# Kernel optimization log

Hardware: AMD Instinct MI355X
Metric: run time of the kernel (lower is better)

Reference implementation:

```python
import jax, jax.numpy as jnp
import numpy as np

B, C, H, W = 4, 512, 64, 64
RED = 8
D = max(1, C // RED)  # inter_channels = 64
BN_EPS = 1e-5


def conv1x1(x, w, b):
    # x: [B,Cin,H,W], w: [Cout,Cin], b: [Cout]
    return jnp.einsum('oc,bchw->bohw', w, x) + b[None, :, None, None]


def setup_inputs() -> dict:
    key = jax.random.key(0)
    ks = jax.random.split(key, 12)
    s = 0.02
    return {
        'x': jax.random.normal(ks[0], (B, C, H, W), jnp.float32),
        'theta_w': jax.random.normal(ks[1], (D, C), jnp.float32) * s,
        'theta_b': jax.random.normal(ks[2], (D,), jnp.float32) * s,
        'phi_w': jax.random.normal(ks[3], (D, C), jnp.float32) * s,
        'phi_b': jax.random.normal(ks[4], (D,), jnp.float32) * s,
        'g_w': jax.random.normal(ks[5], (D, C), jnp.float32) * s,
        'g_b': jax.random.normal(ks[6], (D,), jnp.float32) * s,
        'out_w': jax.random.normal(ks[7], (C, D), jnp.float32) * s,
        'out_b': jax.random.normal(ks[8], (C,), jnp.float32) * s,
        'bn_gamma': jnp.ones((C,), jnp.float32),
        'bn_beta': jnp.zeros((C,), jnp.float32),
        'scale': jax.random.normal(ks[9], (1,), jnp.float32) * 0.1,
    }


def reference(x, theta_w, theta_b, phi_w, phi_b, g_w, g_b,
              out_w, out_b, bn_gamma, bn_beta, scale):
    b, c, h, w = x.shape
    n = h * w
    theta = conv1x1(x, theta_w, theta_b).reshape(b, D, n)  # [B,D,N]
    phi = conv1x1(x, phi_w, phi_b).reshape(b, D, n)        # [B,D,N]
    g = conv1x1(x, g_w, g_b).reshape(b, D, n)              # [B,D,N]
    # attention[b,i,j] = sum_d theta[b,d,i] * phi[b,d,j] (unscaled)
    attn = jax.nn.softmax(jnp.einsum('bdi,bdj->bij', theta, phi), axis=-1)
    # y[b,d,i] = sum_j g[b,d,j] * attn[b,i,j]
    y = jnp.einsum('bdj,bij->bdi', g, attn).reshape(b, D, h, w)
    y = conv1x1(y, out_w, out_b)  # [B,C,H,W]
    # BatchNorm2d, training-mode batch statistics over (B,H,W)
    mean = jnp.mean(y, axis=(0, 2, 3), keepdims=True)
    var = jnp.var(y, axis=(0, 2, 3), keepdims=True)
    y = (y - mean) * jax.lax.rsqrt(var + BN_EPS)
    y = y * bn_gamma[None, :, None, None] + bn_beta[None, :, None, None]
    return x + scale.reshape(()) * y
```

## Files before the change

### kernel.cpp

```cpp
#include <hip/hip_runtime.h>
#include <hip/hip_bf16.h>
#include <math.h>

#define NPIX 4096
#define CIN  512
#define DD   64
#define BB   4
#define NCHUNK 8

using f32x4  = __attribute__((ext_vector_type(4))) float;
using bf16x8 = __attribute__((ext_vector_type(8))) short;
using u16x4  = __attribute__((ext_vector_type(4))) unsigned short;

__device__ __forceinline__ unsigned short f2bf(float f){
    union { __hip_bfloat16 h; unsigned short u; } v;
    v.h = __float2bfloat16(f);
    return v.u;
}

__device__ __forceinline__ float bf2f(unsigned short u){
    union { unsigned u; float f; } v; v.u = ((unsigned)u) << 16; return v.f;
}

__device__ __forceinline__ unsigned pk2(float a, float b){
    union { __hip_bfloat162 h; unsigned u; } v;
    v.h = __float22bfloat162_rn(make_float2(a, b));
    return v.u;
}

__device__ __forceinline__ bf16x8 cvt8(float4 a, float4 b){
    union { unsigned u[4]; bf16x8 v; } r;
    r.u[0] = pk2(a.x, a.y); r.u[1] = pk2(a.z, a.w);
    r.u[2] = pk2(b.x, b.y); r.u[3] = pk2(b.z, b.w);
    return r.v;
}

__global__ __launch_bounds__(256) void k0_xt(
    const float* __restrict__ x, unsigned short* __restrict__ xT)
{
    const int n0 = blockIdx.x * 64;
    const int c0 = blockIdx.y * 64;
    const int b  = blockIdx.z;
    const int tid = threadIdx.x;
    __shared__ __align__(16) unsigned short T[64*72];

    {
        const int kr = tid >> 2, ns = (tid & 3) * 16;
        const float* xp = x + ((size_t)b*CIN + c0 + kr)*NPIX + n0 + ns;
        float4 a0 = *reinterpret_cast<const float4*>(xp);
        float4 a1 = *reinterpret_cast<const float4*>(xp + 4);
        float4 a2 = *reinterpret_cast<const float4*>(xp + 8);
        float4 a3 = *reinterpret_cast<const float4*>(xp + 12);
        *reinterpret_cast<bf16x8*>(&T[kr*72 + ns])     = cvt8(a0, a1);
        *reinterpret_cast<bf16x8*>(&T[kr*72 + ns + 8]) = cvt8(a2, a3);
    }
    __syncthreads();
    {
        const int nr = tid >> 2, ks = (tid & 3) * 16;
        unsigned short v[16];
        #pragma unroll
        for (int i=0;i<16;++i) v[i] = T[(ks+i)*72 + nr];
        unsigned short* dst = xT + ((size_t)b*NPIX + n0 + nr)*CIN + c0 + ks;
        *reinterpret_cast<bf16x8*>(dst)     = *reinterpret_cast<bf16x8*>(&v[0]);
        *reinterpret_cast<bf16x8*>(dst + 8) = *reinterpret_cast<bf16x8*>(&v[8]);
    }
}

__global__ __launch_bounds__(256, 4) void k1_qkv(
    const unsigned short* __restrict__ xT,
    const float* __restrict__ tw, const float* __restrict__ tbv,
    const float* __restrict__ pw, const float* __restrict__ pbv,
    const float* __restrict__ gw, const float* __restrict__ gbv,
    unsigned short* __restrict__ thetaT, unsigned short* __restrict__ phiT,
    unsigned short* __restrict__ g_dn)
{
    const int n0 = blockIdx.x * 64;
    const int kt = blockIdx.y;
    const int b  = blockIdx.z;
    const int tid = threadIdx.x;
    const float* W  = (kt==0) ? tw  : (kt==1) ? pw  : gw;
    const float* Bv = (kt==0) ? tbv : (kt==1) ? pbv : gbv;
    const float wsc = (kt==0) ? 1.4426950408889634f : 1.0f;

    const int wq   = tid >> 6;
    const int lane = tid & 63;
    const int lr   = lane & 15;
    const int lg   = lane >> 4;

    __shared__ __align__(16) short Wt[64*72];
    __shared__ __align__(16) short Xt[64*72];

    f32x4 acc[4];
    #pragma unroll
    for (int jt=0;jt<4;++jt) acc[jt] = (f32x4){0.f,0.f,0.f,0.f};

    const int srow = tid >> 2;
    const int skq  = (tid & 3) * 16;

    for (int k0 = 0; k0 < CIN; k0 += 64) {
        __syncthreads();
        {
            const float* wp = W + (size_t)srow*CIN + k0 + skq;
            float4 w0 = *reinterpret_cast<const float4*>(wp);
            float4 w1 = *reinterpret_cast<const float4*>(wp + 4);
            float4 w2 = *reinterpret_cast<const float4*>(wp + 8);
            float4 w3 = *reinterpret_cast<const float4*>(wp + 12);
            w0.x*=wsc; w0.y*=wsc; w0.z*=wsc; w0.w*=wsc;
            w1.x*=wsc; w1.y*=wsc; w1.z*=wsc; w1.w*=wsc;
            w2.x*=wsc; w2.y*=wsc; w2.z*=wsc; w2.w*=wsc;
            w3.x*=wsc; w3.y*=wsc; w3.z*=wsc; w3.w*=wsc;
            *reinterpret_cast<bf16x8*>(&Wt[srow*72 + skq])     = cvt8(w0, w1);
            *reinterpret_cast<bf16x8*>(&Wt[srow*72 + skq + 8]) = cvt8(w2, w3);
            const unsigned short* xp = xT + ((size_t)b*NPIX + n0 + srow)*CIN + k0 + skq;
            *reinterpret_cast<bf16x8*>(&Xt[srow*72 + skq]) =
                *reinterpret_cast<const bf16x8*>(xp);
            *reinterpret_cast<bf16x8*>(&Xt[srow*72 + skq + 8]) =
                *reinterpret_cast<const bf16x8*>(xp + 8);
        }
        __syncthreads();

        __builtin_amdgcn_s_setprio(1);
        #pragma unroll
        for (int dc=0;dc<2;++dc){
            bf16x8 af = *reinterpret_cast<const bf16x8*>(&Wt[(wq*16+lr)*72 + dc*32 + lg*8]);
            #pragma unroll
            for (int jt=0;jt<4;++jt){
                bf16x8 bf = *reinterpret_cast<const bf16x8*>(&Xt[(jt*16+lr)*72 + dc*32 + lg*8]);
                acc[jt] = __builtin_amdgcn_mfma_f32_16x16x32_bf16(af, bf, acc[jt], 0,0,0);
            }
        }
        __builtin_amdgcn_s_setprio(0);
    }

    const int mb = wq*16 + lg*4;
    float bv[4];
    #pragma unroll
    for (int r=0;r<4;++r) bv[r] = Bv[mb+r] * wsc;

    if (kt < 2){
        unsigned short* dst = (kt==0) ? thetaT : phiT;
        #pragma unroll
        for (int jt=0;jt<4;++jt){
            union { unsigned u[2]; u16x4 v; } o;
            o.u[0] = pk2(acc[jt][0]+bv[0], acc[jt][1]+bv[1]);
            o.u[1] = pk2(acc[jt][2]+bv[2], acc[jt][3]+bv[3]);
            *reinterpret_cast<u16x4*>(&dst[((size_t)b*NPIX + n0 + jt*16+lr)*DD + mb]) = o.v;
        }
    } else {
        #pragma unroll
        for (int jt=0;jt<4;++jt)
            #pragma unroll
            for (int r=0;r<4;++r)
                g_dn[((size_t)b*DD + mb+r)*NPIX + n0 + jt*16+lr] = f2bf(acc[jt][r]+bv[r]);
    }
}

__global__ __launch_bounds__(256, 4) void k2_attn(
    const unsigned short* __restrict__ thetaT,
    const unsigned short* __restrict__ phiT,
    const unsigned short* __restrict__ g_dn,
    unsigned short* __restrict__ pY, float* __restrict__ pL)
{
    const int i0 = blockIdx.x * 128;
    const int ch = blockIdx.y;
    const int b  = blockIdx.z;
    const int tid  = threadIdx.x;
    const int wq   = tid >> 6;
    const int lane = tid & 63;
    const int lr   = lane & 15;
    const int lg   = lane >> 4;

    __shared__ __align__(16) short Kt[64*72];
    __shared__ __align__(16) short Gt[64*72];
    __shared__ __align__(16) short Pb[4*32*72];
    short* Pw = &Pb[wq*32*72];

    bf16x8 qf0[2], qf1[2];
    {
        const unsigned short* qp0 = thetaT + ((size_t)b*NPIX + i0 + wq*16 + lr)*DD + lg*8;
        qf0[0] = *reinterpret_cast<const bf16x8*>(qp0);
        qf0[1] = *reinterpret_cast<const bf16x8*>(qp0 + 32);
        const unsigned short* qp1 = qp0 + (size_t)64*DD;
        qf1[0] = *reinterpret_cast<const bf16x8*>(qp1);
        qf1[1] = *reinterpret_cast<const bf16x8*>(qp1 + 32);
    }
    const bf16x8 onesf = { (short)0x3F80,(short)0x3F80,(short)0x3F80,(short)0x3F80,
                           (short)0x3F80,(short)0x3F80,(short)0x3F80,(short)0x3F80 };

    f32x4 yacc0[4], yacc1[4], lacc0, lacc1;
    #pragma unroll
    for (int dt=0;dt<4;++dt){
        yacc0[dt] = (f32x4){0.f,0.f,0.f,0.f};
        yacc1[dt] = (f32x4){0.f,0.f,0.f,0.f};
    }
    lacc0 = (f32x4){0.f,0.f,0.f,0.f};
    lacc1 = (f32x4){0.f,0.f,0.f,0.f};

    const unsigned short* phb = phiT + (size_t)b*NPIX*DD;
    const unsigned short* gb  = g_dn + (size_t)b*DD*NPIX;

    const int jbeg = ch * (NPIX / NCHUNK);
    const int jend = jbeg + (NPIX / NCHUNK);

    const int srow = tid >> 3;
    const int scb  = (tid & 7) * 8;

    for (int j0 = jbeg; j0 < jend; j0 += 64) {
        __syncthreads();
        *reinterpret_cast<float4*>(&Kt[srow*72 + scb]) =
            *reinterpret_cast<const float4*>(&phb[(size_t)(j0+srow)*DD + scb]);
        *reinterpret_cast<float4*>(&Kt[(srow+32)*72 + scb]) =
            *reinterpret_cast<const float4*>(&phb[(size_t)(j0+srow+32)*DD + scb]);
        *reinterpret_cast<float4*>(&Gt[srow*72 + scb]) =
            *reinterpret_cast<const float4*>(&gb[(size_t)srow*NPIX + j0 + scb]);
        *reinterpret_cast<float4*>(&Gt[(srow+32)*72 + scb]) =
            *reinterpret_cast<const float4*>(&gb[(size_t)(srow+32)*NPIX + j0 + scb]);
        __syncthreads();

        f32x4 s0[4], s1[4];
        #pragma unroll
        for (int jt=0;jt<4;++jt){
            s0[jt] = (f32x4){0.f,0.f,0.f,0.f};
            s1[jt] = (f32x4){0.f,0.f,0.f,0.f};
        }
        __builtin_amdgcn_s_setprio(1);
        #pragma unroll
        for (int dc=0;dc<2;++dc){
            #pragma unroll
            for (int jt=0;jt<4;++jt){
                bf16x8 bf = *reinterpret_cast<const bf16x8*>(&Kt[(jt*16+lr)*72 + dc*32 + lg*8]);
                s0[jt] = __builtin_amdgcn_mfma_f32_16x16x32_bf16(qf0[dc], bf, s0[jt], 0,0,0);
                s1[jt] = __builtin_amdgcn_mfma_f32_16x16x32_bf16(qf1[dc], bf, s1[jt], 0,0,0);
            }
        }
        __builtin_amdgcn_s_setprio(0);

        #pragma unroll
        for (int jt=0;jt<4;++jt)
            #pragma unroll
            for (int r=0;r<4;++r){
                Pw[(lg*4+r)*72      + jt*16 + lr] = (short)f2bf(exp2f(fminf(s0[jt][r], 86.f)));
                Pw[(16+lg*4+r)*72   + jt*16 + lr] = (short)f2bf(exp2f(fminf(s1[jt][r], 86.f)));
            }

        __builtin_amdgcn_s_setprio(1);
        #pragma unroll
        for (int jc=0;jc<2;++jc){
            bf16x8 af0 = *reinterpret_cast<const bf16x8*>(&Pw[lr*72      + jc*32 + lg*8]);
            bf16x8 af1 = *reinterpret_cast<const bf16x8*>(&Pw[(16+lr)*72 + jc*32 + lg*8]);
            #pragma unroll
            for (int dt=0;dt<4;++dt){
                bf16x8 gf = *reinterpret_cast<const bf16x8*>(&Gt[(dt*16+lr)*72 + jc*32 + lg*8]);
                yacc0[dt] = __builtin_amdgcn_mfma_f32_16x16x32_bf16(af0, gf, yacc0[dt], 0,0,0);
                yacc1[dt] = __builtin_amdgcn_mfma_f32_16x16x32_bf16(af1, gf, yacc1[dt], 0,0,0);
            }
            lacc0 = __builtin_amdgcn_mfma_f32_16x16x32_bf16(af0, onesf, lacc0, 0,0,0);
            lacc1 = __builtin_amdgcn_mfma_f32_16x16x32_bf16(af1, onesf, lacc1, 0,0,0);
        }
        __builtin_amdgcn_s_setprio(0);
    }

    {
        unsigned short* py0 = pY + (((size_t)b*NCHUNK + ch)*NPIX + i0 + wq*16)*DD;
        unsigned short* py1 = py0 + (size_t)64*DD;
        #pragma unroll
        for (int r=0;r<4;++r)
            #pragma unroll
            for (int dt=0;dt<4;++dt){
                py0[(size_t)(lg*4+r)*DD + dt*16 + lr] = f2bf(yacc0[dt][r]);
                py1[(size_t)(lg*4+r)*DD + dt*16 + lr] = f2bf(yacc1[dt][r]);
            }
        if (lr == 0){
            const size_t base = ((size_t)b*NCHUNK + ch)*NPIX + i0 + wq*16;
            #pragma unroll
            for (int r=0;r<4;++r){
                pL[base + lg*4+r]      = lacc0[r];
                pL[base + 64 + lg*4+r] = lacc1[r];
            }
        }
    }
}

__global__ __launch_bounds__(256) void k2c_combine(
    const unsigned short* __restrict__ pY, const float* __restrict__ pL,
    unsigned short* __restrict__ yTb)
{
    const int gid = blockIdx.x*256 + threadIdx.x;
    const int d2 = gid & 31;
    const int qn = gid >> 5;
    const int b  = qn >> 12;
    const int i  = qn & (NPIX-1);

    float lsum = 0.f, y0 = 0.f, y1 = 0.f;
    #pragma unroll
    for (int c=0;c<NCHUNK;++c){
        lsum += pL[((size_t)b*NCHUNK + c)*NPIX + i];
        ushort2 v = *reinterpret_cast<const ushort2*>(
            &pY[(((size_t)b*NCHUNK + c)*NPIX + i)*DD + d2*2]);
        y0 += bf2f(v.x); y1 += bf2f(v.y);
    }
    float inv = 1.f / lsum;
    *reinterpret_cast<unsigned*>(&yTb[(size_t)qn*DD + d2*2]) = pk2(y0*inv, y1*inv);
}

__global__ __launch_bounds__(256) void k3_out(
    const unsigned short* __restrict__ yTb, const float* __restrict__ ow,
    const float* __restrict__ ob, float* __restrict__ y2,
    float* __restrict__ psum, float* __restrict__ qsum)
{
    const int n0 = blockIdx.x * 64;
    const int c0 = blockIdx.y * 64;
    const int b  = blockIdx.z;
    const int tid = threadIdx.x;
    const int wq   = tid >> 6;
    const int lane = tid & 63;
    const int lr   = lane & 15;
    const int lg   = lane >> 4;

    __shared__ __align__(16) short Ot[64*72];
    __shared__ __align__(16) short Yt[64*72];

    {
        const int srow = tid >> 2, skq = (tid & 3) * 16;
        const float* wp = ow + (size_t)(c0+srow)*DD + skq;
        float4 w0 = *reinterpret_cast<const float4*>(wp);
        float4 w1 = *reinterpret_cast<const float4*>(wp + 4);
        float4 w2 = *reinterpret_cast<const float4*>(wp + 8);
        float4 w3 = *reinterpret_cast<const float4*>(wp + 12);
        *reinterpret_cast<bf16x8*>(&Ot[srow*72 + skq])     = cvt8(w0, w1);
        *reinterpret_cast<bf16x8*>(&Ot[srow*72 + skq + 8]) = cvt8(w2, w3);
        const unsigned short* yp = yTb + ((size_t)b*NPIX + n0 + srow)*DD + skq;
        *reinterpret_cast<bf16x8*>(&Yt[srow*72 + skq]) =
            *reinterpret_cast<const bf16x8*>(yp);
        *reinterpret_cast<bf16x8*>(&Yt[srow*72 + skq + 8]) =
            *reinterpret_cast<const bf16x8*>(yp + 8);
    }
    __syncthreads();

    f32x4 acc[4];
    #pragma unroll
    for (int jt=0;jt<4;++jt) acc[jt] = (f32x4){0.f,0.f,0.f,0.f};
    #pragma unroll
    for (int dc=0;dc<2;++dc){
        bf16x8 af = *reinterpret_cast<const bf16x8*>(&Ot[(wq*16+lr)*72 + dc*32 + lg*8]);
        #pragma unroll
        for (int jt=0;jt<4;++jt){
            bf16x8 bf = *reinterpret_cast<const bf16x8*>(&Yt[(jt*16+lr)*72 + dc*32 + lg*8]);
            acc[jt] = __builtin_amdgcn_mfma_f32_16x16x32_bf16(af, bf, acc[jt], 0,0,0);
        }
    }

    const int cb = c0 + wq*16 + lg*4;
    float bv[4];
    #pragma unroll
    for (int r=0;r<4;++r) bv[r] = ob[cb+r];

    float sr[4] = {0,0,0,0}, qr[4] = {0,0,0,0};
    #pragma unroll
    for (int jt=0;jt<4;++jt)
        #pragma unroll
        for (int r=0;r<4;++r){
            float v = acc[jt][r] + bv[r];
            y2[((size_t)b*CIN + cb+r)*NPIX + n0 + jt*16+lr] = v;
            sr[r] += v; qr[r] += v*v;
        }
    #pragma unroll
    for (int off=1; off<16; off<<=1)
        #pragma unroll
        for (int r=0;r<4;++r){
            sr[r] += __shfl_xor(sr[r], off);
            qr[r] += __shfl_xor(qr[r], off);
        }
    if (lr == 0){
        const int slot = b*64 + blockIdx.x;
        #pragma unroll
        for (int r=0;r<4;++r){
            psum[(size_t)(cb+r)*256 + slot] = sr[r];
            qsum[(size_t)(cb+r)*256 + slot] = qr[r];
        }
    }
}

__global__ __launch_bounds__(256) void k3b_stats(
    const float* __restrict__ psum, const float* __restrict__ qsum,
    float* __restrict__ meanA, float* __restrict__ invA)
{
    const int c = blockIdx.x;
    const int tid = threadIdx.x;
    float s = psum[(size_t)c*256 + tid];
    float q = qsum[(size_t)c*256 + tid];
    __shared__ float rs[256], rq[256];
    rs[tid]=s; rq[tid]=q; __syncthreads();
    for (int off=128; off; off>>=1){
        if (tid<off){ rs[tid]+=rs[tid+off]; rq[tid]+=rq[tid+off]; }
        __syncthreads();
    }
    if (tid==0){
        const float n = (float)(BB*NPIX);
        float mm = rs[0] / n;
        float v = rq[0] / n - mm*mm;
        meanA[c]=mm; invA[c]=rsqrtf(v + 1e-5f);
    }
}

__global__ __launch_bounds__(256) void k4_final(
    const float* __restrict__ x,
    const float* __restrict__ meanA, const float* __restrict__ invA,
    const float* __restrict__ gamma, const float* __restrict__ beta,
    const float* __restrict__ scale, float* out )
{
    const float sc = scale[0];
    const int total4 = BB*CIN*NPIX/4;
    for (int i4 = blockIdx.x*blockDim.x + threadIdx.x; i4 < total4;
         i4 += gridDim.x*blockDim.x){
        int c = (i4 >> 10) & (CIN-1);
        float4 xv = reinterpret_cast<const float4*>(x)[i4];
        float4 yv = reinterpret_cast<float4*>(out)[i4];
        float mm = meanA[c], iv = invA[c], g = gamma[c], bt = beta[c];
        float4 o;
        o.x = xv.x + sc*(g*(yv.x-mm)*iv + bt);
        o.y = xv.y + sc*(g*(yv.y-mm)*iv + bt);
        o.z = xv.z + sc*(g*(yv.z-mm)*iv + bt);
        o.w = xv.w + sc*(g*(yv.w-mm)*iv + bt);
        reinterpret_cast<float4*>(out)[i4] = o;
    }
}

extern "C" void kernel_launch(void* const* d_in, const int* in_sizes, int n_in,
                              void* d_out, int out_size, void* d_ws, size_t ws_size,
                              hipStream_t stream)
{
    const float* x     = (const float*)d_in[0];
    const float* tw    = (const float*)d_in[1];
    const float* tbv   = (const float*)d_in[2];
    const float* pw    = (const float*)d_in[3];
    const float* pbv   = (const float*)d_in[4];
    const float* gw    = (const float*)d_in[5];
    const float* gbv   = (const float*)d_in[6];
    const float* ow    = (const float*)d_in[7];
    const float* ob    = (const float*)d_in[8];
    const float* gamma = (const float*)d_in[9];
    const float* beta  = (const float*)d_in[10];
    const float* scale = (const float*)d_in[11];
    float* out = (float*)d_out;

    char* wsb = (char*)d_ws;
    unsigned short* thetaT = (unsigned short*)(wsb);
    unsigned short* phiT   = (unsigned short*)(wsb + 2097152);
    unsigned short* g_dn   = (unsigned short*)(wsb + 4194304);
    unsigned short* yTb    = (unsigned short*)(wsb + 6291456);
    float*          pL     = (float*)(wsb + 8388608);
    float*          psum   = (float*)(wsb + 8912896);
    float*          qsum   = (float*)(wsb + 9437184);
    float*          meanA  = (float*)(wsb + 9961472);
    float*          invA   = (float*)(wsb + 9963520);

    unsigned short* xT = (unsigned short*)d_out;
    unsigned short* pY = (unsigned short*)d_out;
    float* y2 = out;

    k0_xt  <<<dim3(64,8,4), 256, 0, stream>>>(x, xT);
    k1_qkv <<<dim3(64,3,4), 256, 0, stream>>>(xT, tw, tbv, pw, pbv, gw, gbv,
                                              thetaT, phiT, g_dn);
    k2_attn<<<dim3(32,NCHUNK,4), 256, 0, stream>>>(thetaT, phiT, g_dn, pY, pL);
    k2c_combine<<<2048, 256, 0, stream>>>(pY, pL, yTb);
    k3_out <<<dim3(64,8,4), 256, 0, stream>>>(yTb, ow, ob, y2, psum, qsum);
    k3b_stats<<<512, 256, 0, stream>>>(psum, qsum, meanA, invA);
    k4_final<<<2048, 256, 0, stream>>>(x, meanA, invA, gamma, beta, scale, out);
}
```

Measured before the change: 96.71 us.

## Load K/G fragments directly from global in attention; store out-conv result as bf16

The attention kernel drops its shared-memory staging of phi and g tiles. Each wave now loads its MFMA operand fragments straight from global memory into registers, which removes two block barriers per tile; the occupancy hint is lowered to 3 to make room for the extra registers. Separately, the output-projection result is written as bf16 to a workspace buffer instead of fp32 into the output, which halves the traffic for that intermediate in the final normalization pass. The trade-offs are redundant global loads across the four waves, with no cross-wave reuse through LDS, and a loss of precision in the pre-BatchNorm values.

```diff
diff --git a/kernel.cpp b/kernel.cpp
--- a/kernel.cpp
+++ b/kernel.cpp
@@ -155,7 +155,7 @@
     }
 }
 
-__global__ __launch_bounds__(256, 4) void k2_attn(
+__global__ __launch_bounds__(256, 3) void k2_attn(
     const unsigned short* __restrict__ thetaT,
     const unsigned short* __restrict__ phiT,
     const unsigned short* __restrict__ g_dn,
@@ -170,8 +170,6 @@
     const int lr   = lane & 15;
     const int lg   = lane >> 4;
 
-    __shared__ __align__(16) short Kt[64*72];
-    __shared__ __align__(16) short Gt[64*72];
     __shared__ __align__(16) short Pb[4*32*72];
     short* Pw = &Pb[wq*32*72];
 
@@ -202,20 +200,14 @@
     const int jbeg = ch * (NPIX / NCHUNK);
     const int jend = jbeg + (NPIX / NCHUNK);
 
-    const int srow = tid >> 3;
-    const int scb  = (tid & 7) * 8;
-
     for (int j0 = jbeg; j0 < jend; j0 += 64) {
-        __syncthreads();
-        *reinterpret_cast<float4*>(&Kt[srow*72 + scb]) =
-            *reinterpret_cast<const float4*>(&phb[(size_t)(j0+srow)*DD + scb]);
-        *reinterpret_cast<float4*>(&Kt[(srow+32)*72 + scb]) =
-            *reinterpret_cast<const float4*>(&phb[(size_t)(j0+srow+32)*DD + scb]);
-        *reinterpret_cast<float4*>(&Gt[srow*72 + scb]) =
-            *reinterpret_cast<const float4*>(&gb[(size_t)srow*NPIX + j0 + scb]);
-        *reinterpret_cast<float4*>(&Gt[(srow+32)*72 + scb]) =
-            *reinterpret_cast<const float4*>(&gb[(size_t)(srow+32)*NPIX + j0 + scb]);
-        __syncthreads();
+        bf16x8 kf[2][4];
+        #pragma unroll
+        for (int jt=0;jt<4;++jt){
+            const unsigned short* kp = phb + (size_t)(j0 + jt*16 + lr)*DD + lg*8;
+            kf[0][jt] = *reinterpret_cast<const bf16x8*>(kp);
+            kf[1][jt] = *reinterpret_cast<const bf16x8*>(kp + 32);
+        }
 
         f32x4 s0[4], s1[4];
         #pragma unroll
@@ -228,19 +220,26 @@
         for (int dc=0;dc<2;++dc){
             #pragma unroll
             for (int jt=0;jt<4;++jt){
-                bf16x8 bf = *reinterpret_cast<const bf16x8*>(&Kt[(jt*16+lr)*72 + dc*32 + lg*8]);
-                s0[jt] = __builtin_amdgcn_mfma_f32_16x16x32_bf16(qf0[dc], bf, s0[jt], 0,0,0);
-                s1[jt] = __builtin_amdgcn_mfma_f32_16x16x32_bf16(qf1[dc], bf, s1[jt], 0,0,0);
+                s0[jt] = __builtin_amdgcn_mfma_f32_16x16x32_bf16(qf0[dc], kf[dc][jt], s0[jt], 0,0,0);
+                s1[jt] = __builtin_amdgcn_mfma_f32_16x16x32_bf16(qf1[dc], kf[dc][jt], s1[jt], 0,0,0);
             }
         }
         __builtin_amdgcn_s_setprio(0);
 
+        bf16x8 gf[2][4];
+        #pragma unroll
+        for (int jc=0;jc<2;++jc)
+            #pragma unroll
+            for (int dt=0;dt<4;++dt)
+                gf[jc][dt] = *reinterpret_cast<const bf16x8*>(
+                    gb + (size_t)(dt*16+lr)*NPIX + j0 + jc*32 + lg*8);
+
         #pragma unroll
         for (int jt=0;jt<4;++jt)
             #pragma unroll
             for (int r=0;r<4;++r){
-                Pw[(lg*4+r)*72      + jt*16 + lr] = (short)f2bf(exp2f(fminf(s0[jt][r], 86.f)));
-                Pw[(16+lg*4+r)*72   + jt*16 + lr] = (short)f2bf(exp2f(fminf(s1[jt][r], 86.f)));
+                Pw[(lg*4+r)*72    + jt*16 + lr] = (short)f2bf(exp2f(fminf(s0[jt][r], 86.f)));
+                Pw[(16+lg*4+r)*72 + jt*16 + lr] = (short)f2bf(exp2f(fminf(s1[jt][r], 86.f)));
             }
 
         __builtin_amdgcn_s_setprio(1);
@@ -250,9 +249,8 @@
             bf16x8 af1 = *reinterpret_cast<const bf16x8*>(&Pw[(16+lr)*72 + jc*32 + lg*8]);
             #pragma unroll
             for (int dt=0;dt<4;++dt){
-                bf16x8 gf = *reinterpret_cast<const bf16x8*>(&Gt[(dt*16+lr)*72 + jc*32 + lg*8]);
-                yacc0[dt] = __builtin_amdgcn_mfma_f32_16x16x32_bf16(af0, gf, yacc0[dt], 0,0,0);
-                yacc1[dt] = __builtin_amdgcn_mfma_f32_16x16x32_bf16(af1, gf, yacc1[dt], 0,0,0);
+                yacc0[dt] = __builtin_amdgcn_mfma_f32_16x16x32_bf16(af0, gf[jc][dt], yacc0[dt], 0,0,0);
+                yacc1[dt] = __builtin_amdgcn_mfma_f32_16x16x32_bf16(af1, gf[jc][dt], yacc1[dt], 0,0,0);
             }
             lacc0 = __builtin_amdgcn_mfma_f32_16x16x32_bf16(af0, onesf, lacc0, 0,0,0);
             lacc1 = __builtin_amdgcn_mfma_f32_16x16x32_bf16(af1, onesf, lacc1, 0,0,0);
@@ -305,7 +303,7 @@
 
 __global__ __launch_bounds__(256) void k3_out(
     const unsigned short* __restrict__ yTb, const float* __restrict__ ow,
-    const float* __restrict__ ob, float* __restrict__ y2,
+    const float* __restrict__ ob, unsigned short* __restrict__ y2b,
     float* __restrict__ psum, float* __restrict__ qsum)
 {
     const int n0 = blockIdx.x * 64;
@@ -361,7 +359,7 @@
         #pragma unroll
         for (int r=0;r<4;++r){
             float v = acc[jt][r] + bv[r];
-            y2[((size_t)b*CIN + cb+r)*NPIX + n0 + jt*16+lr] = v;
+            y2b[((size_t)b*CIN + cb+r)*NPIX + n0 + jt*16+lr] = f2bf(v);
             sr[r] += v; qr[r] += v*v;
         }
     #pragma unroll
@@ -404,10 +402,10 @@
 }
 
 __global__ __launch_bounds__(256) void k4_final(
-    const float* __restrict__ x,
+    const float* __restrict__ x, const unsigned short* __restrict__ y2b,
     const float* __restrict__ meanA, const float* __restrict__ invA,
     const float* __restrict__ gamma, const float* __restrict__ beta,
-    const float* __restrict__ scale, float* out )
+    const float* __restrict__ scale, float* __restrict__ out)
 {
     const float sc = scale[0];
     const int total4 = BB*CIN*NPIX/4;
@@ -415,13 +413,13 @@
          i4 += gridDim.x*blockDim.x){
         int c = (i4 >> 10) & (CIN-1);
         float4 xv = reinterpret_cast<const float4*>(x)[i4];
-        float4 yv = reinterpret_cast<float4*>(out)[i4];
+        ushort4 yv = reinterpret_cast<const ushort4*>(y2b)[i4];
         float mm = meanA[c], iv = invA[c], g = gamma[c], bt = beta[c];
         float4 o;
-        o.x = xv.x + sc*(g*(yv.x-mm)*iv + bt);
-        o.y = xv.y + sc*(g*(yv.y-mm)*iv + bt);
-        o.z = xv.z + sc*(g*(yv.z-mm)*iv + bt);
-        o.w = xv.w + sc*(g*(yv.w-mm)*iv + bt);
+        o.x = xv.x + sc*(g*(bf2f(yv.x)-mm)*iv + bt);
+        o.y = xv.y + sc*(g*(bf2f(yv.y)-mm)*iv + bt);
+        o.z = xv.z + sc*(g*(bf2f(yv.z)-mm)*iv + bt);
+        o.w = xv.w + sc*(g*(bf2f(yv.w)-mm)*iv + bt);
         reinterpret_cast<float4*>(out)[i4] = o;
     }
 }
@@ -454,17 +452,17 @@
     float*          qsum   = (float*)(wsb + 9437184);
     float*          meanA  = (float*)(wsb + 9961472);
     float*          invA   = (float*)(wsb + 9963520);
+    unsigned short* y2b    = (unsigned short*)(wsb + 16777216);
 
     unsigned short* xT = (unsigned short*)d_out;
     unsigned short* pY = (unsigned short*)d_out;
-    float* y2 = out;
 
     k0_xt  <<<dim3(64,8,4), 256, 0, stream>>>(x, xT);
     k1_qkv <<<dim3(64,3,4), 256, 0, stream>>>(xT, tw, tbv, pw, pbv, gw, gbv,
                                               thetaT, phiT, g_dn);
     k2_attn<<<dim3(32,NCHUNK,4), 256, 0, stream>>>(thetaT, phiT, g_dn, pY, pL);
     k2c_combine<<<2048, 256, 0, stream>>>(pY, pL, yTb);
-    k3_out <<<dim3(64,8,4), 256, 0, stream>>>(yTb, ow, ob, y2, psum, qsum);
+    k3_out <<<dim3(64,8,4), 256, 0, stream>>>(yTb, ow, ob, y2b, psum, qsum);
     k3b_stats<<<512, 256, 0, stream>>>(psum, qsum, meanA, invA);
-    k4_final<<<2048, 256, 0, stream>>>(x, meanA, invA, gamma, beta, scale, out);
-}
+    k4_final<<<2048, 256, 0, stream>>>(x, y2b, meanA, invA, gamma, beta, scale, out);
+}
```

Result: slower. 127.4 us (+31.7%).
